# Kernel optimization log

Hardware: AMD Instinct MI355X
Metric: run time of the kernel (lower is better)

## Reference

```python
import jax, jax.numpy as jnp
import numpy as np

B, T, D = 4, 4096, 768
N = 256           # events per doc
HID = 200


def setup_inputs() -> dict:
    key = jax.random.key(0)
    k = jax.random.split(key, 8)
    event_embed = jax.random.normal(k[0], (B, T, D), dtype=jnp.float32)
    event_idx = jax.random.randint(k[1], (B, N), 0, T)
    W1 = jax.random.normal(k[2], (3 * D, HID), dtype=jnp.float32) * 0.02
    b1 = jnp.zeros((HID,), jnp.float32)
    W2 = jax.random.normal(k[3], (HID, HID), dtype=jnp.float32) * 0.02
    b2 = jnp.zeros((HID,), jnp.float32)
    W3 = jax.random.normal(k[4], (HID, 1), dtype=jnp.float32) * 0.02
    b3 = jnp.zeros((1,), jnp.float32)
    return {"event_embed": event_embed, "event_idx": event_idx,
            "W1": W1, "b1": b1, "W2": W2, "b2": b2, "W3": W3, "b3": b3}


def reference(event_embed, event_idx, W1, b1, W2, b2, W3, b3):
    n = event_idx.shape[1]
    # gather event embeddings: [B, N, D]
    emb = jnp.take_along_axis(event_embed, event_idx[..., None], axis=1)
    # all ordered pairs (i, j) with j < i (antecedents)
    ii, jj = jnp.tril_indices(n, k=-1)          # each [P], P = N(N-1)/2
    i_g = emb[:, ii, :]                          # [B, P, D]
    j_g = emb[:, jj, :]
    pairs = jnp.concatenate((i_g, j_g, i_g * j_g), axis=-1)   # [B, P, 3D]
    # 3-layer MLP score (dropout is identity in eval mode)
    h = jax.nn.relu(jnp.einsum('bpe,eh->bph', pairs, W1) + b1)
    h = jax.nn.relu(jnp.einsum('bph,hk->bpk', h, W2) + b2)
    s = (jnp.einsum('bph,ho->bpo', h, W3) + b3)[..., 0]        # [B, P]
    # scatter into score matrix; diagonal = epsilon score 0.0
    S = jnp.zeros((emb.shape[0], n, n), dtype=s.dtype)
    S = S.at[:, ii, jj].set(s)
    valid = (jnp.arange(n)[None, :] <= jnp.arange(n)[:, None])  # j <= i
    logits = jnp.where(valid[None], S, -jnp.inf)
    probs = jax.nn.softmax(logits, axis=-1)                    # row-wise softmax
    return jnp.where(valid[None], probs, jnp.float32(-1000.0))  # pad value -1000
```

## Files before the change

### kernel.cpp

```cpp
#include <hip/hip_runtime.h>


#define NB 4
#define NN 256
#define DD 768
#define TT 4096
#define HP 224
#define NTILES 14
#define KT1 24
#define KT2 7
#define TRI 136
#define ABS 448
#define MTS 3584

typedef _Float16 f16x8 __attribute__((ext_vector_type(8)));
typedef _Float16 f16x2 __attribute__((ext_vector_type(2)));
typedef __attribute__((ext_vector_type(4))) float f32x4;

union FragU { uint4 u; f16x8 h; };
union H2U { unsigned int u; f16x2 h; };

__device__ __forceinline__ unsigned int h2mul(unsigned int a, unsigned int b) {
    H2U x, y, r; x.u = a; y.u = b; r.h = x.h * y.h;
    return r.u;
}
__device__ __forceinline__ float hlo(unsigned int v) { H2U x; x.u = v; return (float)x.h[0]; }
__device__ __forceinline__ float hhi(unsigned int v) { H2U x; x.u = v; return (float)x.h[1]; }
__device__ __forceinline__ unsigned short f2h(float f) {
    _Float16 h = (_Float16)f;
    union { _Float16 h; unsigned short u; } r; r.h = h; return r.u;
}
__device__ __forceinline__ float h2f(unsigned short u) {
    union { unsigned short u; _Float16 h; } r; r.u = u; return (float)r.h;
}
__device__ __forceinline__ unsigned int packh(float lo, float hi) {
    return ((unsigned int)f2h(hi) << 16) | (unsigned int)f2h(lo);
}

__global__ void prep_all(const float* __restrict__ W1, const float* __restrict__ W2,
                         const float* __restrict__ ee, const int* __restrict__ eidx,
                         unsigned short* __restrict__ w1n,
                         unsigned short* __restrict__ w1s,
                         unsigned short* __restrict__ w2s,
                         unsigned short* __restrict__ emb) {
    const int N1n8 = 24 * 28 * 64;
    const int N1s8 = 24 * 14 * 64;
    const int N28  = 7 * 14 * 64;
    int bx = blockIdx.x;
    if (bx >= 277) {
        int tid = threadIdx.x;
        int m = (bx - 277) * 4 + (tid >> 6);
        int lane = tid & 63;
        int b = m >> 8, n = m & 255;
        int t = eidx[b * NN + n];
        const float* src = ee + ((size_t)b * TT + t) * DD;
        uint4* dst = (uint4*)(emb + ((size_t)b * NN + n) * DD);
        for (int chunk = lane; chunk < 96; chunk += 64) {
            const float4* s4 = (const float4*)(src + chunk * 8);
            float4 lo4 = s4[0], hi4 = s4[1];
            uint4 o;
            o.x = packh(lo4.x, lo4.y); o.y = packh(lo4.z, lo4.w);
            o.z = packh(hi4.x, hi4.y); o.w = packh(hi4.z, hi4.w);
            dst[chunk] = o;
        }
        return;
    }
    int idx8 = bx * 256 + threadIdx.x;
    if (idx8 < N1n8) {
        int lane = idx8 & 63, f = idx8 >> 6;
        int nt = f % 28, kt = f / 28;
        int k0 = kt * 32 + ((lane >> 4) << 3);
        int n = nt * 16 + (lane & 15);
        unsigned int o[4];
#pragma unroll
        for (int jp = 0; jp < 4; ++jp) {
            float v0, v1;
            int ka = k0 + 2 * jp, kb = ka + 1;
            if (n < HP) {
                v0 = (n < 200) ? W1[(size_t)ka * 200 + n] : 0.f;
                v1 = (n < 200) ? W1[(size_t)kb * 200 + n] : 0.f;
            } else {
                int c2 = n - HP;
                v0 = (c2 < 200) ? W1[(size_t)(768 + ka) * 200 + c2] : 0.f;
                v1 = (c2 < 200) ? W1[(size_t)(768 + kb) * 200 + c2] : 0.f;
            }
            o[jp] = packh(v0, v1);
        }
        *(uint4*)&w1n[(size_t)idx8 * 8] = make_uint4(o[0], o[1], o[2], o[3]);
    } else if (idx8 < N1n8 + N1s8) {
        int i2 = idx8 - N1n8;
        int lane = i2 & 63, f = i2 >> 6;
        int nt = f % NTILES, kt = f / NTILES;
        int k0 = kt * 32 + ((lane >> 4) << 3);
        int n = nt * 16 + (lane & 15);
        unsigned int o[4];
#pragma unroll
        for (int jp = 0; jp < 4; ++jp) {
            int ka = k0 + 2 * jp, kb = ka + 1;
            float v0 = (n < 200) ? W1[(size_t)(1536 + ka) * 200 + n] : 0.f;
            float v1 = (n < 200) ? W1[(size_t)(1536 + kb) * 200 + n] : 0.f;
            o[jp] = packh(v0, v1);
        }
        *(uint4*)&w1s[(size_t)i2 * 8] = make_uint4(o[0], o[1], o[2], o[3]);
    } else if (idx8 < N1n8 + N1s8 + N28) {
        int i2 = idx8 - N1n8 - N1s8;
        int lane = i2 & 63, f = i2 >> 6;
        int nt = f % NTILES, kt = f / NTILES;
        int k0 = kt * 32 + ((lane >> 4) << 3);
        int n = nt * 16 + (lane & 15);
        unsigned int o[4];
#pragma unroll
        for (int jp = 0; jp < 4; ++jp) {
            int ka = k0 + 2 * jp, kb = ka + 1;
            float v0 = (ka < 200 && n < 200) ? W2[(size_t)ka * 200 + n] : 0.f;
            float v1 = (kb < 200 && n < 200) ? W2[(size_t)kb * 200 + n] : 0.f;
            o[jp] = packh(v0, v1);
        }
        *(uint4*)&w2s[(size_t)i2 * 8] = make_uint4(o[0], o[1], o[2], o[3]);
    }
}

__global__ __launch_bounds__(64)
void node_mfma(const unsigned short* __restrict__ emb,
               const unsigned short* __restrict__ w1n,
               unsigned short* __restrict__ AB) {
    int lane = threadIdx.x & 63;
    int q = lane >> 4, c = lane & 15;
    int mt = blockIdx.x >> 2;
    int ng = blockIdx.x & 3;
    int m0 = mt * 16;
    const uint4* ga = (const uint4*)emb + (size_t)(m0 + c) * 96;
    const uint4* gb = (const uint4*)w1n;

    f32x4 acc[7];
#pragma unroll
    for (int n = 0; n < 7; ++n) acc[n] = (f32x4){0.f, 0.f, 0.f, 0.f};

    uint4 aA, aB, bA[7], bB[7];
    aA = ga[q];
#pragma unroll
    for (int n = 0; n < 7; ++n) bA[n] = gb[((0 * 28 + ng * 7 + n) << 6) + lane];

#pragma unroll 1
    for (int kt = 0; kt < KT1; kt += 2) {
        aB = ga[(kt + 1) * 4 + q];
#pragma unroll
        for (int n = 0; n < 7; ++n) bB[n] = gb[(((kt + 1) * 28 + ng * 7 + n) << 6) + lane];
        {
            FragU a; a.u = aA;
#pragma unroll
            for (int n = 0; n < 7; ++n) {
                FragU bb; bb.u = bA[n];
                acc[n] = __builtin_amdgcn_mfma_f32_16x16x32_f16(a.h, bb.h, acc[n], 0, 0, 0);
            }
        }
        if (kt + 2 < KT1) {
            aA = ga[(kt + 2) * 4 + q];
#pragma unroll
            for (int n = 0; n < 7; ++n) bA[n] = gb[(((kt + 2) * 28 + ng * 7 + n) << 6) + lane];
        }
        {
            FragU a; a.u = aB;
#pragma unroll
            for (int n = 0; n < 7; ++n) {
                FragU bb; bb.u = bB[n];
                acc[n] = __builtin_amdgcn_mfma_f32_16x16x32_f16(a.h, bb.h, acc[n], 0, 0, 0);
            }
        }
    }
#pragma unroll
    for (int n = 0; n < 7; ++n) {
        int col = (ng * 7 + n) * 16 + c;
#pragma unroll
        for (int rr = 0; rr < 4; ++rr)
            AB[(size_t)(m0 + q * 4 + rr) * ABS + col] = f2h(acc[n][rr]);
    }
}

__global__ __launch_bounds__(128, 2)
void pair_wave(
    const unsigned short* __restrict__ emb,
    const unsigned short* __restrict__ w1s,
    const unsigned short* __restrict__ w2s,
    const unsigned short* __restrict__ AB,
    const float* __restrict__ b1, const float* __restrict__ b2,
    const float* __restrict__ W3, const float* __restrict__ b3,
    float* __restrict__ S) {
    int bid = blockIdx.x;
    int rp = bid / 544;
    int g = bid % 544;
    int b = g / TRI;
    int r = g % TRI;
    int ti = (int)((sqrtf(8.f * (float)r + 1.f) - 1.f) * 0.5f);
    while ((ti + 1) * (ti + 2) / 2 <= r) ++ti;
    while (ti * (ti + 1) / 2 > r) --ti;
    int tj = r - ti * (ti + 1) / 2;
    int i0 = ti << 4, j0 = tj << 4;

    int tid = threadIdx.x;
    int lane = tid & 63;
    int nh = tid >> 6;
    int q = lane >> 4, c = lane & 15;
    int iA = i0 + rp * 4;

    __shared__ __align__(16) unsigned short smH[4 * MTS];
    __shared__ float sred[2][64];

    const uint4* w1f = (const uint4*)w1s;
    const uint4* w2f = (const uint4*)w2s;
    const uint4* gI[4];
#pragma unroll
    for (int t = 0; t < 4; ++t)
        gI[t] = (const uint4*)(emb + ((size_t)b * NN + iA + t) * DD);
    const uint4* gJc = (const uint4*)(emb + ((size_t)b * NN + j0 + c) * DD);

    f32x4 acc[4][7];
#pragma unroll
    for (int t = 0; t < 4; ++t)
#pragma unroll
        for (int n = 0; n < 7; ++n)
            acc[t][n] = (f32x4){0.f, 0.f, 0.f, 0.f};

    {
        uint4 bfrA[7], bfrB[7];
        uint4 ejA, ejB, eA[4], eB[4];
#pragma unroll
        for (int n = 0; n < 7; ++n) bfrA[n] = w1f[(nh * 7 + n) * 64 + lane];
        ejA = gJc[q];
#pragma unroll
        for (int t = 0; t < 4; ++t) eA[t] = gI[t][q];

#pragma unroll 1
        for (int kt = 0; kt < KT1; kt += 2) {
#pragma unroll
            for (int n = 0; n < 7; ++n)
                bfrB[n] = w1f[((kt + 1) * NTILES + nh * 7 + n) * 64 + lane];
            ejB = gJc[(kt + 1) * 4 + q];
#pragma unroll
            for (int t = 0; t < 4; ++t) eB[t] = gI[t][(kt + 1) * 4 + q];
            __builtin_amdgcn_s_setprio(1);
#pragma unroll
            for (int t = 0; t < 4; ++t) {
                FragU a;
                a.u.x = h2mul(eA[t].x, ejA.x); a.u.y = h2mul(eA[t].y, ejA.y);
                a.u.z = h2mul(eA[t].z, ejA.z); a.u.w = h2mul(eA[t].w, ejA.w);
#pragma unroll
                for (int n = 0; n < 7; ++n) {
                    FragU bb; bb.u = bfrA[n];
                    acc[t][n] = __builtin_amdgcn_mfma_f32_16x16x32_f16(a.h, bb.h, acc[t][n], 0, 0, 0);
                }
            }
            __builtin_amdgcn_s_setprio(0);
            if (kt + 2 < KT1) {
#pragma unroll
                for (int n = 0; n < 7; ++n)
                    bfrA[n] = w1f[((kt + 2) * NTILES + nh * 7 + n) * 64 + lane];
                ejA = gJc[(kt + 2) * 4 + q];
#pragma unroll
                for (int t = 0; t < 4; ++t) eA[t] = gI[t][(kt + 2) * 4 + q];
            }
            __builtin_amdgcn_s_setprio(1);
#pragma unroll
            for (int t = 0; t < 4; ++t) {
                FragU a;
                a.u.x = h2mul(eB[t].x, ejB.x); a.u.y = h2mul(eB[t].y, ejB.y);
                a.u.z = h2mul(eB[t].z, ejB.z); a.u.w = h2mul(eB[t].w, ejB.w);
#pragma unroll
                for (int n = 0; n < 7; ++n) {
                    FragU bb; bb.u = bfrB[n];
                    acc[t][n] = __builtin_amdgcn_mfma_f32_16x16x32_f16(a.h, bb.h, acc[t][n], 0, 0, 0);
                }
            }
            __builtin_amdgcn_s_setprio(0);
        }
    }

    {
        unsigned int bvp[7][2];
#pragma unroll
        for (int n = 0; n < 7; ++n) {
            int h = ((nh * 7 + n) << 4) + c;
#pragma unroll
            for (int p = 0; p < 2; ++p) {
                unsigned int lo = AB[((size_t)b * NN + j0 + q * 4 + 2 * p) * ABS + HP + h];
                unsigned int hi = AB[((size_t)b * NN + j0 + q * 4 + 2 * p + 1) * ABS + HP + h];
                bvp[n][p] = (hi << 16) | lo;
            }
        }
#pragma unroll
        for (int t = 0; t < 4; ++t) {
            unsigned short* slot = &smH[t * MTS];
#pragma unroll
            for (int n = 0; n < 7; ++n) {
                int h = ((nh * 7 + n) << 4) + c;
                float b1v = (h < 200) ? b1[h] : 0.f;
                float af = h2f(AB[((size_t)b * NN + iA + t) * ABS + h]) + b1v;
                int kk2 = h >> 5, q2 = (h >> 3) & 3, j2 = h & 7;
                int fa = ((kk2 * 4 + q2) << 7) + j2;
#pragma unroll
                for (int rr = 0; rr < 4; ++rr) {
                    float bvf = (rr & 1) ? hhi(bvp[n][rr >> 1]) : hlo(bvp[n][rr >> 1]);
                    slot[fa + ((q * 4 + rr) << 3)] =
                        f2h(fmaxf(acc[t][n][rr] + af + bvf, 0.f));
                }
            }
        }
    }
    __syncthreads();

    f32x4 acc2[4][7];
#pragma unroll
    for (int t = 0; t < 4; ++t)
#pragma unroll
        for (int n = 0; n < 7; ++n)
            acc2[t][n] = (f32x4){0.f, 0.f, 0.f, 0.f};

    {
        uint4 bfrA[7], bfrB[7];
#pragma unroll
        for (int n = 0; n < 7; ++n) bfrA[n] = w2f[(nh * 7 + n) * 64 + lane];

#pragma unroll 1
        for (int kk = 0; kk < 6; kk += 2) {
#pragma unroll
            for (int n = 0; n < 7; ++n)
                bfrB[n] = w2f[((kk + 1) * NTILES + nh * 7 + n) * 64 + lane];
            __builtin_amdgcn_s_setprio(1);
#pragma unroll
            for (int t = 0; t < 4; ++t) {
                FragU a2;
                a2.u = *(const uint4*)(&smH[t * MTS + (((kk * 4 + q) * 16 + c) << 3)]);
#pragma unroll
                for (int n = 0; n < 7; ++n) {
                    FragU bb; bb.u = bfrA[n];
                    acc2[t][n] = __builtin_amdgcn_mfma_f32_16x16x32_f16(a2.h, bb.h, acc2[t][n], 0, 0, 0);
                }
            }
            __builtin_amdgcn_s_setprio(0);
#pragma unroll
            for (int n = 0; n < 7; ++n)
                bfrA[n] = w2f[((kk + 2) * NTILES + nh * 7 + n) * 64 + lane];
            __builtin_amdgcn_s_setprio(1);
#pragma unroll
            for (int t = 0; t < 4; ++t) {
                FragU a2;
                a2.u = *(const uint4*)(&smH[t * MTS + ((((kk + 1) * 4 + q) * 16 + c) << 3)]);
#pragma unroll
                for (int n = 0; n < 7; ++n) {
                    FragU bb; bb.u = bfrB[n];
                    acc2[t][n] = __builtin_amdgcn_mfma_f32_16x16x32_f16(a2.h, bb.h, acc2[t][n], 0, 0, 0);
                }
            }
            __builtin_amdgcn_s_setprio(0);
        }
        __builtin_amdgcn_s_setprio(1);
#pragma unroll
        for (int t = 0; t < 4; ++t) {
            FragU a2;
            a2.u = *(const uint4*)(&smH[t * MTS + (((6 * 4 + q) * 16 + c) << 3)]);
#pragma unroll
            for (int n = 0; n < 7; ++n) {
                FragU bb; bb.u = bfrA[n];
                acc2[t][n] = __builtin_amdgcn_mfma_f32_16x16x32_f16(a2.h, bb.h, acc2[t][n], 0, 0, 0);
            }
        }
        __builtin_amdgcn_s_setprio(0);
    }

    {
        float b2v[7], w3v[7];
#pragma unroll
        for (int n = 0; n < 7; ++n) {
            int h = ((nh * 7 + n) << 4) + c;
            b2v[n] = (h < 200) ? b2[h] : 0.f;
            w3v[n] = (h < 200) ? W3[h] : 0.f;
        }
#pragma unroll
        for (int t = 0; t < 4; ++t) {
#pragma unroll
            for (int rr = 0; rr < 4; ++rr) {
                float part = 0.f;
#pragma unroll
                for (int n = 0; n < 7; ++n) {
                    float hv = fmaxf(acc2[t][n][rr] + b2v[n], 0.f);
                    part += hv * w3v[n];
                }
                part += __shfl_xor(part, 1);
                part += __shfl_xor(part, 2);
                part += __shfl_xor(part, 4);
                part += __shfl_xor(part, 8);
                if (c == 0)
                    sred[nh][t * 16 + q * 4 + rr] = part;
            }
        }
    }
    __syncthreads();

    if (tid < 64) {
        int t = tid >> 4, jj = tid & 15;
        float s = sred[0][tid] + sred[1][tid] + b3[0];
        S[((size_t)b * NN + iA + t) * NN + j0 + jj] = s;
    }
}

__global__ __launch_bounds__(256) void softmax_rows(const float* __restrict__ S,
                                                    float* __restrict__ out) {
    int b = blockIdx.x >> 8, i = blockIdx.x & 255;
    int j = threadIdx.x;
    int lane = j & 63, w = j >> 6;
    __shared__ float red[16];
    float x = (j < i) ? S[((size_t)b * NN + i) * NN + j] : ((j == i) ? 0.f : -1e30f);
    float m = x;
#pragma unroll
    for (int off = 32; off; off >>= 1) m = fmaxf(m, __shfl_xor(m, off));
    if (lane == 0) red[w] = m;
    __syncthreads();
    float mx = fmaxf(fmaxf(red[0], red[1]), fmaxf(red[2], red[3]));
    float e = (j <= i) ? __expf(x - mx) : 0.f;
    float s = e;
#pragma unroll
    for (int off = 32; off; off >>= 1) s += __shfl_xor(s, off);
    if (lane == 0) red[8 + w] = s;
    __syncthreads();
    float sum = red[8] + red[9] + red[10] + red[11];
    out[((size_t)b * NN + i) * NN + j] = (j <= i) ? (e / sum) : -1000.0f;
}

extern "C" void kernel_launch(void* const* d_in, const int* in_sizes, int n_in,
                              void* d_out, int out_size, void* d_ws, size_t ws_size,
                              hipStream_t stream) {
    const float* ee  = (const float*)d_in[0];
    const int*   eidx = (const int*)d_in[1];
    const float* W1  = (const float*)d_in[2];
    const float* b1  = (const float*)d_in[3];
    const float* W2  = (const float*)d_in[4];
    const float* b2  = (const float*)d_in[5];
    const float* W3  = (const float*)d_in[6];
    const float* b3  = (const float*)d_in[7];
    float* out = (float*)d_out;

    char* p = (char*)d_ws;
    unsigned short* emb = (unsigned short*)p; p += (size_t)NB * NN * DD * 2;
    unsigned short* w1n = (unsigned short*)p; p += (size_t)24 * 28 * 512 * 2;
    unsigned short* w1s = (unsigned short*)p; p += (size_t)24 * 14 * 512 * 2;
    unsigned short* w2s = (unsigned short*)p; p += (size_t)7 * 14 * 512 * 2;
    unsigned short* AB  = (unsigned short*)p; p += (size_t)NB * NN * ABS * 2;
    float* S  = (float*)p; p += (size_t)NB * NN * NN * 4;

    prep_all<<<533, 256, 0, stream>>>(W1, W2, ee, eidx, w1n, w1s, w2s, emb);
    node_mfma<<<256, 64, 0, stream>>>(emb, w1n, AB);
    pair_wave<<<2176, 128, 0, stream>>>(emb, w1s, w2s, AB, b1, b2, W3, b3, S);
    softmax_rows<<<NB * NN, 256, 0, stream>>>(S, out);
}
```

Measured before the change: 204.1 us.

## Stream W1 fragments through triple-buffered LDS via global_load_lds

The first-layer weight fragments were loaded from global memory straight into registers, double-buffered. They are now copied asynchronously into a per-wave triple-buffered LDS region with global_load_lds, using hand-placed vmcnt waits, and read from LDS just before the MFMAs. The aim is to take weight loads off the register path and hide their latency further ahead of use. It adds about 42 KB of LDS, which may lower occupancy, and relies on fragile manual vmcnt counting.

```diff
diff --git a/kernel.cpp b/kernel.cpp
--- a/kernel.cpp
+++ b/kernel.cpp
@@ -12,6 +12,7 @@
 #define TRI 136
 #define ABS 448
 #define MTS 3584
+#define WSH 3584
 
 typedef _Float16 f16x8 __attribute__((ext_vector_type(8)));
 typedef _Float16 f16x2 __attribute__((ext_vector_type(2)));
@@ -35,6 +36,11 @@
 }
 __device__ __forceinline__ unsigned int packh(float lo, float hi) {
     return ((unsigned int)f2h(hi) << 16) | (unsigned int)f2h(lo);
+}
+__device__ __forceinline__ void gload_lds16(const unsigned short* g, unsigned short* l) {
+    __builtin_amdgcn_global_load_lds(
+        (const __attribute__((address_space(1))) unsigned int*)g,
+        (__attribute__((address_space(3))) unsigned int*)l, 16, 0, 0);
 }
 
 __global__ void prep_all(const float* __restrict__ W1, const float* __restrict__ W2,
@@ -204,9 +210,10 @@
     int iA = i0 + rp * 4;
 
     __shared__ __align__(16) unsigned short smH[4 * MTS];
+    __shared__ __align__(16) unsigned short smW[2 * 3 * WSH];
     __shared__ float sred[2][64];
-
-    const uint4* w1f = (const uint4*)w1s;
+    unsigned short* myW = &smW[nh * 3 * WSH];
+
     const uint4* w2f = (const uint4*)w2s;
     const uint4* gI[4];
 #pragma unroll
@@ -214,6 +221,13 @@
         gI[t] = (const uint4*)(emb + ((size_t)b * NN + iA + t) * DD);
     const uint4* gJc = (const uint4*)(emb + ((size_t)b * NN + j0 + c) * DD);
 
+    auto stageW = [&](int kt, int bsel) {
+#pragma unroll
+        for (int n = 0; n < 7; ++n)
+            gload_lds16(w1s + ((size_t)((kt * NTILES + nh * 7 + n) * 64) + lane) * 8,
+                        myW + bsel * WSH + n * 512 + lane * 8);
+    };
+
     f32x4 acc[4][7];
 #pragma unroll
     for (int t = 0; t < 4; ++t)
@@ -222,19 +236,27 @@
             acc[t][n] = (f32x4){0.f, 0.f, 0.f, 0.f};
 
     {
-        uint4 bfrA[7], bfrB[7];
         uint4 ejA, ejB, eA[4], eB[4];
-#pragma unroll
-        for (int n = 0; n < 7; ++n) bfrA[n] = w1f[(nh * 7 + n) * 64 + lane];
+        stageW(0, 0);
+        stageW(1, 1);
         ejA = gJc[q];
 #pragma unroll
         for (int t = 0; t < 4; ++t) eA[t] = gI[t][q];
 
+        int b0 = 0;
 #pragma unroll 1
         for (int kt = 0; kt < KT1; kt += 2) {
-#pragma unroll
-            for (int n = 0; n < 7; ++n)
-                bfrB[n] = w1f[((kt + 1) * NTILES + nh * 7 + n) * 64 + lane];
+            int b1 = b0 + 1; if (b1 > 2) b1 -= 3;
+            int b2 = b1 + 1; if (b2 > 2) b2 -= 3;
+            if (kt == 0) asm volatile("s_waitcnt vmcnt(12)" ::: "memory");
+            else         asm volatile("s_waitcnt vmcnt(17)" ::: "memory");
+            uint4 bfrA[7];
+            {
+                const uint4* wf = (const uint4*)(myW + b0 * WSH);
+#pragma unroll
+                for (int n = 0; n < 7; ++n) bfrA[n] = wf[n * 64 + lane];
+            }
+            if (kt + 2 < KT1) stageW(kt + 2, b2);
             ejB = gJc[(kt + 1) * 4 + q];
 #pragma unroll
             for (int t = 0; t < 4; ++t) eB[t] = gI[t][(kt + 1) * 4 + q];
@@ -251,10 +273,17 @@
                 }
             }
             __builtin_amdgcn_s_setprio(0);
+            if (kt == 22) asm volatile("s_waitcnt vmcnt(10)" ::: "memory");
+            else          asm volatile("s_waitcnt vmcnt(17)" ::: "memory");
+            uint4 bfrB[7];
+            {
+                const uint4* wf = (const uint4*)(myW + b1 * WSH);
+#pragma unroll
+                for (int n = 0; n < 7; ++n) bfrB[n] = wf[n * 64 + lane];
+            }
+            asm volatile("" ::: "memory");
+            if (kt + 3 < KT1) stageW(kt + 3, b0);
             if (kt + 2 < KT1) {
-#pragma unroll
-                for (int n = 0; n < 7; ++n)
-                    bfrA[n] = w1f[((kt + 2) * NTILES + nh * 7 + n) * 64 + lane];
                 ejA = gJc[(kt + 2) * 4 + q];
 #pragma unroll
                 for (int t = 0; t < 4; ++t) eA[t] = gI[t][(kt + 2) * 4 + q];
@@ -272,6 +301,7 @@
                 }
             }
             __builtin_amdgcn_s_setprio(0);
+            b0 = b2;
         }
     }
 
```

Measured after the change: 246.7 us. 20.9% more time.

## Fuse row softmax into pair kernel via per-row completion counters

Applied to the files above, without the earlier changes.

Removes the separate softmax launch. Each pair block stores its scores atomically, then bumps a per-row counter, and the last block to finish a row computes that row's softmax and writes the output directly. This saves a kernel launch and the extra read of S from a separate pass. In exchange it adds a memset, atomics, and serialized softmax work in the tail blocks, whose extra __syncthreads may lengthen those blocks.

```diff
diff --git a/kernel.cpp b/kernel.cpp
--- a/kernel.cpp
+++ b/kernel.cpp
@@ -185,7 +185,7 @@
     const unsigned short* __restrict__ AB,
     const float* __restrict__ b1, const float* __restrict__ b2,
     const float* __restrict__ W3, const float* __restrict__ b3,
-    float* __restrict__ S) {
+    float* __restrict__ S, int* __restrict__ cnt, float* __restrict__ out) {
     int bid = blockIdx.x;
     int rp = bid / 544;
     int g = bid % 544;
@@ -205,6 +205,9 @@
 
     __shared__ __align__(16) unsigned short smH[4 * MTS];
     __shared__ float sred[2][64];
+    __shared__ int rowsF[4];
+    __shared__ int nfS;
+    __shared__ float smax[2], ssum[2];
 
     const uint4* w1f = (const uint4*)w1s;
     const uint4* w2f = (const uint4*)w2s;
@@ -399,31 +402,47 @@
     if (tid < 64) {
         int t = tid >> 4, jj = tid & 15;
         float s = sred[0][tid] + sred[1][tid] + b3[0];
-        S[((size_t)b * NN + iA + t) * NN + j0 + jj] = s;
-    }
-}
-
-__global__ __launch_bounds__(256) void softmax_rows(const float* __restrict__ S,
-                                                    float* __restrict__ out) {
-    int b = blockIdx.x >> 8, i = blockIdx.x & 255;
-    int j = threadIdx.x;
-    int lane = j & 63, w = j >> 6;
-    __shared__ float red[16];
-    float x = (j < i) ? S[((size_t)b * NN + i) * NN + j] : ((j == i) ? 0.f : -1e30f);
-    float m = x;
-#pragma unroll
-    for (int off = 32; off; off >>= 1) m = fmaxf(m, __shfl_xor(m, off));
-    if (lane == 0) red[w] = m;
+        __hip_atomic_store(&S[((size_t)b * NN + iA + t) * NN + j0 + jj], s,
+                           __ATOMIC_RELAXED, __HIP_MEMORY_SCOPE_AGENT);
+    }
+    if (tid == 0) nfS = 0;
     __syncthreads();
-    float mx = fmaxf(fmaxf(red[0], red[1]), fmaxf(red[2], red[3]));
-    float e = (j <= i) ? __expf(x - mx) : 0.f;
-    float s = e;
-#pragma unroll
-    for (int off = 32; off; off >>= 1) s += __shfl_xor(s, off);
-    if (lane == 0) red[8 + w] = s;
+
+    if (tid < 4) {
+        int i = iA + tid;
+        int need = (i >> 4) + 1;
+        int old = __hip_atomic_fetch_add(&cnt[b * NN + i], 1,
+                                         __ATOMIC_ACQ_REL, __HIP_MEMORY_SCOPE_AGENT);
+        if (old + 1 == need) rowsF[atomicAdd(&nfS, 1)] = i;
+    }
     __syncthreads();
-    float sum = red[8] + red[9] + red[10] + red[11];
-    out[((size_t)b * NN + i) * NN + j] = (j <= i) ? (e / sum) : -1000.0f;
+
+    for (int f = 0; f < nfS; ++f) {
+        int i = rowsF[f];
+        const float* rowp = &S[((size_t)b * NN + i) * NN];
+        int ja = tid, jb = tid + 128;
+        float va = __hip_atomic_load(&rowp[ja], __ATOMIC_RELAXED, __HIP_MEMORY_SCOPE_AGENT);
+        float vb = __hip_atomic_load(&rowp[jb], __ATOMIC_RELAXED, __HIP_MEMORY_SCOPE_AGENT);
+        float xa = (ja < i) ? va : ((ja == i) ? 0.f : -1e30f);
+        float xb = (jb < i) ? vb : ((jb == i) ? 0.f : -1e30f);
+        float m = fmaxf(xa, xb);
+#pragma unroll
+        for (int off = 32; off; off >>= 1) m = fmaxf(m, __shfl_xor(m, off));
+        if (lane == 0) smax[nh] = m;
+        __syncthreads();
+        float mx = fmaxf(smax[0], smax[1]);
+        float ea = (ja <= i) ? __expf(xa - mx) : 0.f;
+        float eb = (jb <= i) ? __expf(xb - mx) : 0.f;
+        float s = ea + eb;
+#pragma unroll
+        for (int off = 32; off; off >>= 1) s += __shfl_xor(s, off);
+        if (lane == 0) ssum[nh] = s;
+        __syncthreads();
+        float sum = ssum[0] + ssum[1];
+        out[((size_t)b * NN + i) * NN + ja] = (ja <= i) ? (ea / sum) : -1000.0f;
+        out[((size_t)b * NN + i) * NN + jb] = (jb <= i) ? (eb / sum) : -1000.0f;
+        __syncthreads();
+    }
 }
 
 extern "C" void kernel_launch(void* const* d_in, const int* in_sizes, int n_in,
@@ -446,9 +465,10 @@
     unsigned short* w2s = (unsigned short*)p; p += (size_t)7 * 14 * 512 * 2;
     unsigned short* AB  = (unsigned short*)p; p += (size_t)NB * NN * ABS * 2;
     float* S  = (float*)p; p += (size_t)NB * NN * NN * 4;
-
+    int* cnt = (int*)p; p += (size_t)NB * NN * sizeof(int);
+
+    hipMemsetAsync(cnt, 0, (size_t)NB * NN * sizeof(int), stream);
     prep_all<<<533, 256, 0, stream>>>(W1, W2, ee, eidx, w1n, w1s, w2s, emb);
     node_mfma<<<256, 64, 0, stream>>>(emb, w1n, AB);
-    pair_wave<<<2176, 128, 0, stream>>>(emb, w1s, w2s, AB, b1, b2, W3, b3, S);
-    softmax_rows<<<NB * NN, 256, 0, stream>>>(S, out);
-}
+    pair_wave<<<2176, 128, 0, stream>>>(emb, w1s, w2s, AB, b1, b2, W3, b3, S, cnt, out);
+}
```

Measured after the change: 234.7 us. 1.15x slower.
